# Optimization experiments

Measured on AMD Instinct MI355X. Metric: run time of the kernel, lower is better.

Reference implementation:

```python
import jax, jax.numpy as jnp
import numpy as np
from jax import lax

STRIDE = 1
PAD = 1


def setup_inputs() -> dict:
    key = jax.random.key(0)
    k1, k2 = jax.random.split(key)
    X = jax.random.normal(k1, (16, 64, 256, 256), dtype=jnp.float32)
    K = jax.random.normal(k2, (3, 3), dtype=jnp.float32)
    return {"X": X, "K": K}


def reference(X, K):
    # out[b, c, i, j] = sum(patch(X[b, c], i, j) * K)
    # == depthwise conv with a single shared 2D kernel for all channels.
    B, C, H, W = X.shape
    x = X.reshape(B * C, 1, H, W)            # fold channels into batch
    k = K[None, None, :, :]                  # [O=1, I=1, kh, kw]
    out = lax.conv_general_dilated(
        x, k,
        window_strides=(STRIDE, STRIDE),
        padding=[(PAD, PAD), (PAD, PAD)],
        dimension_numbers=("NCHW", "OIHW", "NCHW"),
    )
    Ho, Wo = out.shape[2], out.shape[3]
    return out.reshape(B, C, Ho, Wo)
```

## Files before the change

kernel.cpp:

```cpp
#include <hip/hip_runtime.h>


#define CONV_H 256
#define CONV_W 256
#define CONV_W4 64
#define NPLANES (16 * 64)

__global__ __launch_bounds__(256)
void conv3x3_kernel(const float* __restrict__ X,
                    const float* __restrict__ Kw,
                    float* __restrict__ out)
{
    const float k00 = Kw[0], k01 = Kw[1], k02 = Kw[2];
    const float k10 = Kw[3], k11 = Kw[4], k12 = Kw[5];
    const float k20 = Kw[6], k21 = Kw[7], k22 = Kw[8];

    const int idx = blockIdx.x * blockDim.x + threadIdx.x;
    const int w4 = idx & (CONV_W4 - 1);
    const int h  = (idx >> 6) & (CONV_H - 1);
    const int p  = idx >> 14;

    const float* plane = X + (size_t)p * (CONV_H * CONV_W);
    const int col0 = w4 << 2;

    float acc0 = 0.f, acc1 = 0.f, acc2 = 0.f, acc3 = 0.f;

    #pragma unroll
    for (int dr = -1; dr <= 1; ++dr) {
        const int r = h + dr;
        float4 c = make_float4(0.f, 0.f, 0.f, 0.f);
        float  l = 0.f, rt = 0.f;
        if (r >= 0 && r < CONV_H) {
            const float* rowp = plane + r * CONV_W + col0;
            c = *(const float4*)rowp;
            if (w4 > 0)           l  = rowp[-1];
            if (w4 < CONV_W4 - 1) rt = rowp[4];
        }
        float ka, kb, kc;
        if (dr == -1)      { ka = k00; kb = k01; kc = k02; }
        else if (dr == 0)  { ka = k10; kb = k11; kc = k12; }
        else               { ka = k20; kb = k21; kc = k22; }
        acc0 += ka * l   + kb * c.x + kc * c.y;
        acc1 += ka * c.x + kb * c.y + kc * c.z;
        acc2 += ka * c.y + kb * c.z + kc * c.w;
        acc3 += ka * c.z + kb * c.w + kc * rt;
    }

    *(float4*)(out + (size_t)idx * 4) = make_float4(acc0, acc1, acc2, acc3);
}

extern "C" void kernel_launch(void* const* d_in, const int* in_sizes, int n_in,
                              void* d_out, int out_size, void* d_ws, size_t ws_size,
                              hipStream_t stream) {
    const float* X  = (const float*)d_in[0];
    const float* Kw = (const float*)d_in[1];
    float* out = (float*)d_out;

    const int total_f4 = NPLANES * CONV_H * CONV_W4;
    const int block = 256;
    const int grid = total_f4 / block;
    conv3x3_kernel<<<grid, block, 0, stream>>>(X, Kw, out);
}
```

Before: 452.7 us.

## Process eight rows per thread with rolling row registers and remap blocks

Each thread now computes an 8-row vertical stripe of four output columns, keeping the previous, current and next input rows in registers so each input row is loaded about once instead of three times. Block indices are also permuted across eight chunks, presumably to spread concurrently running blocks across memory channels or XCDs. This cuts redundant loads and the thread count by eight, at the cost of less parallelism and a serial dependency chain per thread.

```diff
diff --git a/kernel.cpp b/kernel.cpp
--- a/kernel.cpp
+++ b/kernel.cpp
@@ -5,6 +5,24 @@
 #define CONV_W 256
 #define CONV_W4 64
 #define NPLANES (16 * 64)
+#define ROWS_PER_THREAD 8
+
+struct Row { float4 c; float l, r; };
+
+__device__ __forceinline__ Row load_row(const float* __restrict__ rowp, int w4) {
+    Row v;
+    v.c = *(const float4*)rowp;
+    v.l = (w4 > 0)            ? rowp[-1] : 0.f;
+    v.r = (w4 < CONV_W4 - 1)  ? rowp[4]  : 0.f;
+    return v;
+}
+
+__device__ __forceinline__ Row zero_row() {
+    Row v;
+    v.c = make_float4(0.f, 0.f, 0.f, 0.f);
+    v.l = 0.f; v.r = 0.f;
+    return v;
+}
 
 __global__ __launch_bounds__(256)
 void conv3x3_kernel(const float* __restrict__ X,
@@ -15,38 +33,47 @@
     const float k10 = Kw[3], k11 = Kw[4], k12 = Kw[5];
     const float k20 = Kw[6], k21 = Kw[7], k22 = Kw[8];
 
-    const int idx = blockIdx.x * blockDim.x + threadIdx.x;
-    const int w4 = idx & (CONV_W4 - 1);
-    const int h  = (idx >> 6) & (CONV_H - 1);
-    const int p  = idx >> 14;
+    const int chunk = gridDim.x >> 3;
+    const int lb = (blockIdx.x & 7) * chunk + (blockIdx.x >> 3);
+
+    const int tid    = lb * blockDim.x + threadIdx.x;
+    const int w4     = tid & (CONV_W4 - 1);
+    const int stripe = tid >> 6;
+    const int h0     = (stripe & 31) << 3;
+    const int p      = stripe >> 5;
 
     const float* plane = X + (size_t)p * (CONV_H * CONV_W);
     const int col0 = w4 << 2;
+    float* outp = out + (size_t)p * (CONV_H * CONV_W) + (size_t)h0 * CONV_W + col0;
 
-    float acc0 = 0.f, acc1 = 0.f, acc2 = 0.f, acc3 = 0.f;
+    Row rm = (h0 > 0) ? load_row(plane + (h0 - 1) * CONV_W + col0, w4) : zero_row();
+    Row rc = load_row(plane + h0 * CONV_W + col0, w4);
 
     #pragma unroll
-    for (int dr = -1; dr <= 1; ++dr) {
-        const int r = h + dr;
-        float4 c = make_float4(0.f, 0.f, 0.f, 0.f);
-        float  l = 0.f, rt = 0.f;
-        if (r >= 0 && r < CONV_H) {
-            const float* rowp = plane + r * CONV_W + col0;
-            c = *(const float4*)rowp;
-            if (w4 > 0)           l  = rowp[-1];
-            if (w4 < CONV_W4 - 1) rt = rowp[4];
-        }
-        float ka, kb, kc;
-        if (dr == -1)      { ka = k00; kb = k01; kc = k02; }
-        else if (dr == 0)  { ka = k10; kb = k11; kc = k12; }
-        else               { ka = k20; kb = k21; kc = k22; }
-        acc0 += ka * l   + kb * c.x + kc * c.y;
-        acc1 += ka * c.x + kb * c.y + kc * c.z;
-        acc2 += ka * c.y + kb * c.z + kc * c.w;
-        acc3 += ka * c.z + kb * c.w + kc * rt;
+    for (int i = 0; i < ROWS_PER_THREAD; ++i) {
+        const int hp = h0 + i + 1;
+        Row rp = (hp < CONV_H) ? load_row(plane + hp * CONV_W + col0, w4)
+                               : zero_row();
+
+        float4 o;
+        o.x = k00 * rm.l   + k01 * rm.c.x + k02 * rm.c.y
+            + k10 * rc.l   + k11 * rc.c.x + k12 * rc.c.y
+            + k20 * rp.l   + k21 * rp.c.x + k22 * rp.c.y;
+        o.y = k00 * rm.c.x + k01 * rm.c.y + k02 * rm.c.z
+            + k10 * rc.c.x + k11 * rc.c.y + k12 * rc.c.z
+            + k20 * rp.c.x + k21 * rp.c.y + k22 * rp.c.z;
+        o.z = k00 * rm.c.y + k01 * rm.c.z + k02 * rm.c.w
+            + k10 * rc.c.y + k11 * rc.c.z + k12 * rc.c.w
+            + k20 * rp.c.y + k21 * rp.c.z + k22 * rp.c.w;
+        o.w = k00 * rm.c.z + k01 * rm.c.w + k02 * rm.r
+            + k10 * rc.c.z + k11 * rc.c.w + k12 * rc.r
+            + k20 * rp.c.z + k21 * rp.c.w + k22 * rp.r;
+
+        *(float4*)(outp + i * CONV_W) = o;
+
+        rm = rc;
+        rc = rp;
     }
-
-    *(float4*)(out + (size_t)idx * 4) = make_float4(acc0, acc1, acc2, acc3);
 }
 
 extern "C" void kernel_launch(void* const* d_in, const int* in_sizes, int n_in,
@@ -56,8 +83,8 @@
     const float* Kw = (const float*)d_in[1];
     float* out = (float*)d_out;
 
-    const int total_f4 = NPLANES * CONV_H * CONV_W4;
+    const int total_threads = NPLANES * (CONV_H / ROWS_PER_THREAD) * CONV_W4;
     const int block = 256;
-    const int grid = total_f4 / block;
+    const int grid = total_threads / block;
     conv3x3_kernel<<<grid, block, 0, stream>>>(X, Kw, out);
 }
```

Result: no change. 450.7 us (-0.4%).
